# Performance work log

Measured on AMD Instinct MI355X. Metric: run time of the kernel, lower is better.

Reference implementation:

```python
import jax, jax.numpy as jnp
import numpy as np

B, T, D, H = 256, 200, 256, 4
ITEMS = 100000
ALPHA = 0.5
L = 4          # num_blocks: first L//2 causal layers, last L//2 decoder layers
EPS = 1e-8


def _ln(x, s, b):
    m = x.mean(-1, keepdims=True)
    v = ((x - m) ** 2).mean(-1, keepdims=True)
    return (x - m) / jnp.sqrt(v + EPS) * s + b


def _encoder(x, attn_mask, causal_mask, p):
    ln1_s, ln1_b, Wq, bq, Wk, bk, Wv, bv, Wo, bo, ln2_s, ln2_b, W1, b1, W2, b2 = p
    dk = D // H
    Q = _ln(x, ln1_s, ln1_b)
    # attn(Q, seqs, seqs): q from normed input, k/v from raw input
    q = (Q @ Wq + bq).reshape(B, T, H, dk).transpose(0, 2, 1, 3)
    k = (x @ Wk + bk).reshape(B, T, H, dk).transpose(0, 2, 1, 3)
    v = (x @ Wv + bv).reshape(B, T, H, dk).transpose(0, 2, 1, 3)
    scores = jnp.einsum('bhqd,bhkd->bhqk', q, k) / jnp.sqrt(jnp.float32(dk))
    scores = jnp.where(attn_mask[None, None], jnp.float32(-1e9), scores)
    if causal_mask is not None:  # multiplicative reweighting before softmax
        scores = scores * (1.0 + ALPHA * causal_mask[:, None])
    a = jax.nn.softmax(scores, axis=-1)
    o = jnp.einsum('bhqk,bhkd->bhqd', a, v).transpose(0, 2, 1, 3).reshape(B, T, D)
    s = Q + (o @ Wo + bo)          # residual uses normed Q (as in source)
    y = _ln(s, ln2_s, ln2_b)
    return jax.nn.relu(y @ W1 + b1) @ W2 + b2 + y


def setup_inputs() -> dict:
    key = jax.random.key(0)
    ks = jax.random.split(key, 24)
    w = lambda k, shape: jax.random.normal(k, shape, jnp.float32) * 0.02
    log_seqs = jax.random.randint(ks[0], (B, T), 0, ITEMS + 1)
    item_table = w(ks[1], (ITEMS + 1, D)).at[0].set(0.0)   # padding_idx=0
    pos_table = w(ks[2], (T + 1, D)).at[0].set(0.0)        # maxlen+1 rows
    return dict(
        log_seqs=log_seqs,
        item_table=item_table,
        pos_table=pos_table,
        ln1_s=jnp.ones((L, D), jnp.float32), ln1_b=jnp.zeros((L, D), jnp.float32),
        Wq=w(ks[3], (L, D, D)), bq=w(ks[4], (L, D)),
        Wk=w(ks[5], (L, D, D)), bk=w(ks[6], (L, D)),
        Wv=w(ks[7], (L, D, D)), bv=w(ks[8], (L, D)),
        Wo=w(ks[9], (L, D, D)), bo=w(ks[10], (L, D)),
        ln2_s=jnp.ones((L, D), jnp.float32), ln2_b=jnp.zeros((L, D), jnp.float32),
        W1=w(ks[11], (L, D, D)), b1=w(ks[12], (L, D)),
        W2=w(ks[13], (L, D, D)), b2=w(ks[14], (L, D)),
        last_s=jnp.ones((D,), jnp.float32), last_b=jnp.zeros((D,), jnp.float32),
    )


def reference(log_seqs, item_table, pos_table, ln1_s, ln1_b, Wq, bq, Wk, bk, Wv, bv,
              Wo, bo, ln2_s, ln2_b, W1, b1, W2, b2, last_s, last_b):
    seqs = item_table[log_seqs] * jnp.sqrt(jnp.float32(D))
    poss = jnp.arange(1, T + 1)[None, :] * (log_seqs != 0)
    seqs = seqs + pos_table[poss]
    attn_mask = jnp.triu(jnp.ones((T, T), bool), k=1)  # True above diagonal -> masked

    def p(i):
        return (ln1_s[i], ln1_b[i], Wq[i], bq[i], Wk[i], bk[i], Wv[i], bv[i],
                Wo[i], bo[i], ln2_s[i], ln2_b[i], W1[i], b1[i], W2[i], b2[i])

    # causal layers: each applied to the ORIGINAL seqs (matches repo loop)
    causal_z = seqs
    for i in range(L // 2):
        causal_z = _encoder(seqs, attn_mask, None, p(i))
    # batch_cov of causal_z.permute(0,2,1): points [B, N=D, T] -> cov [B, T, T]
    pts = jnp.swapaxes(causal_z, 1, 2)
    diffs = pts - pts.mean(1, keepdims=True)
    causal_mask = jnp.minimum(jnp.einsum('bnt,bns->bts', diffs, diffs) / (D - 1), 3.0)

    x = seqs
    for i in range(L // 2, L):
        x = _encoder(x, attn_mask, causal_mask, p(i))
    return _ln(x, last_s, last_b)
```

## Files before the change

### kernel.cpp

```cpp
#include <hip/hip_runtime.h>
#include <hip/hip_bf16.h>

#define B_ 256
#define T_ 200
#define D_ 256
#define H_ 4
#define BT_ (B_*T_)
#define DD_ (D_*D_)
#define GS_ 72
#define TP_ 208
#define VTP_ 224
#define ZS_ 264
#define FS_ 264
#define VS_ 136

typedef __attribute__((ext_vector_type(4))) float  f32x4;
typedef __attribute__((ext_vector_type(8))) __bf16 bf16x8;
typedef __attribute__((ext_vector_type(4))) int    i32x4;
typedef __attribute__((ext_vector_type(2))) int    i32x2;

union frag8 { unsigned u[4]; bf16x8 v; };

__device__ __forceinline__ unsigned short f2bf(float f) {
    unsigned u = __float_as_uint(f);
    u += 0x7FFFu + ((u >> 16) & 1u);
    return (unsigned short)(u >> 16);
}
__device__ __forceinline__ unsigned pk2(float lo, float hi) {
    return (unsigned)f2bf(lo) | ((unsigned)f2bf(hi) << 16);
}
__device__ __forceinline__ float bflo(unsigned u) { return __uint_as_float(u << 16); }
__device__ __forceinline__ float bfhi(unsigned u) { return __uint_as_float(u & 0xFFFF0000u); }

__device__ __forceinline__ float wave_sum(float v) {
#pragma unroll
    for (int o = 32; o >= 1; o >>= 1) v += __shfl_xor(v, o);
    return v;
}

__global__ void embed_kernel(const int* __restrict__ ls,
                             const float* __restrict__ itab,
                             const float* __restrict__ ptab,
                             unsigned short* __restrict__ seqs) {
    int bt = blockIdx.x;
    int t = bt % T_;
    int lane = threadIdx.x;
    int idx = ls[bt];
    int pos = idx ? (t + 1) : 0;
    float4 a = ((const float4*)(itab + (size_t)idx * D_))[lane];
    float4 p = ((const float4*)(ptab + (size_t)pos * D_))[lane];
    i32x2 r;
    r[0] = (int)pk2(a.x*16.f+p.x, a.y*16.f+p.y);
    r[1] = (int)pk2(a.z*16.f+p.z, a.w*16.f+p.w);
    ((i32x2*)(seqs + (size_t)bt * D_))[lane] = r;
}

template<bool F32OUT>
__global__ __launch_bounds__(256) void ln_kernel(const unsigned short* __restrict__ X,
                                                 const float* __restrict__ sc,
                                                 const float* __restrict__ bi,
                                                 void* __restrict__ Y) {
    int row = blockIdx.x * 4 + (threadIdx.x >> 6);
    int lane = threadIdx.x & 63;
    i32x2 xv = ((const i32x2*)(X + (size_t)row * D_))[lane];
    float x0 = bflo((unsigned)xv[0]), x1 = bfhi((unsigned)xv[0]);
    float x2 = bflo((unsigned)xv[1]), x3 = bfhi((unsigned)xv[1]);
    float m = wave_sum(x0 + x1 + x2 + x3) * (1.f / D_);
    float d0 = x0 - m, d1 = x1 - m, d2 = x2 - m, d3 = x3 - m;
    float v = wave_sum(d0*d0 + d1*d1 + d2*d2 + d3*d3) * (1.f / D_);
    float inv = rsqrtf(v + 1e-8f);
    float4 s4 = ((const float4*)sc)[lane];
    float4 b4 = ((const float4*)bi)[lane];
    float r0 = d0*inv*s4.x + b4.x, r1 = d1*inv*s4.y + b4.y;
    float r2 = d2*inv*s4.z + b4.z, r3 = d3*inv*s4.w + b4.w;
    if (F32OUT) {
        float4 r = {r0, r1, r2, r3};
        ((float4*)Y)[(size_t)row * (D_/4) + lane] = r;
    } else {
        i32x2 r;
        r[0] = (int)pk2(r0, r1);
        r[1] = (int)pk2(r2, r3);
        ((i32x2*)Y)[(size_t)row * (D_/4) + lane] = r;
    }
}

__global__ __launch_bounds__(256) void wtrans_kernel(const float* __restrict__ W,
                                                     unsigned short* __restrict__ Wt) {
    __shared__ float tile[64][65];
    int c0 = blockIdx.x * 64, r0 = blockIdx.y * 64, l = blockIdx.z;
    const float* src = W + (size_t)l * DD_;
    unsigned short* dst = Wt + (size_t)l * DD_;
    int tid = threadIdx.x;
#pragma unroll
    for (int rep = 0; rep < 16; ++rep) {
        int idx = rep * 256 + tid;
        int r = idx >> 6, c = idx & 63;
        tile[r][c] = src[(size_t)(r0 + r) * D_ + c0 + c];
    }
    __syncthreads();
#pragma unroll
    for (int rep = 0; rep < 16; ++rep) {
        int idx = rep * 256 + tid;
        int r2 = idx >> 6, c2 = idx & 63;
        dst[(size_t)(c0 + r2) * D_ + r0 + c2] = f2bf(tile[c2][r2]);
    }
}

__global__ void vtpad_kernel(unsigned short* __restrict__ vt) {
    if (threadIdx.x < VTP_ - T_)
        vt[(size_t)blockIdx.x * VTP_ + T_ + threadIdx.x] = 0;
}

template<int OM, bool RES>
__global__ __launch_bounds__(256) void gemm_mfma(
    const unsigned short* __restrict__ A, const unsigned short* __restrict__ Wt,
    const float* __restrict__ bias, const unsigned short* res,
    unsigned short* Cout) {
    __shared__ unsigned short sh[2 * 128 * GS_];
    unsigned short* As = sh;
    unsigned short* Ws = sh + 128 * GS_;
    int t = threadIdx.x, lane = t & 63, wv = t >> 6;
    int wm = wv >> 1, wn = wv & 1;
    int l15 = lane & 15, l4 = lane >> 4;
    int m0 = blockIdx.y * 128, n0 = blockIdx.x * 128;

    f32x4 acc[4][4];
#pragma unroll
    for (int m = 0; m < 4; ++m)
#pragma unroll
        for (int n = 0; n < 4; ++n)
            acc[m][n] = f32x4{0.f, 0.f, 0.f, 0.f};

    for (int k0 = 0; k0 < D_; k0 += 64) {
#pragma unroll
        for (int rep = 0; rep < 4; ++rep) {
            int idx = rep * 256 + t;
            int r = idx >> 3, c8 = (idx & 7) * 8;
            *(i32x4*)&As[r * GS_ + c8] =
                *(const i32x4*)(A + (size_t)(m0 + r) * D_ + k0 + c8);
        }
#pragma unroll
        for (int rep = 0; rep < 4; ++rep) {
            int idx = rep * 256 + t;
            int r = idx >> 3, c8 = (idx & 7) * 8;
            *(i32x4*)&Ws[r * GS_ + c8] =
                *(const i32x4*)(Wt + (size_t)(n0 + r) * D_ + k0 + c8);
        }
        __syncthreads();
#pragma unroll
        for (int kk = 0; kk < 2; ++kk) {
            bf16x8 af[4], bf[4];
#pragma unroll
            for (int m = 0; m < 4; ++m)
                af[m] = *(const bf16x8*)&As[(wm*64 + m*16 + l15) * GS_ + kk*32 + l4*8];
#pragma unroll
            for (int n = 0; n < 4; ++n)
                bf[n] = *(const bf16x8*)&Ws[(wn*64 + n*16 + l15) * GS_ + kk*32 + l4*8];
#pragma unroll
            for (int m = 0; m < 4; ++m)
#pragma unroll
                for (int n = 0; n < 4; ++n)
                    acc[m][n] = __builtin_amdgcn_mfma_f32_16x16x32_bf16(af[m], bf[n], acc[m][n], 0, 0, 0);
        }
        __syncthreads();
    }

    unsigned short* Ct = sh;
#pragma unroll
    for (int n = 0; n < 4; ++n) {
        int gnl = wn*64 + n*16 + l15;
        int gn = n0 + gnl;
        float bn = bias[gn];
#pragma unroll
        for (int m = 0; m < 4; ++m) {
#pragma unroll
            for (int i = 0; i < 4; ++i) {
                int gml = wm*64 + m*16 + l4*4 + i;
                int gm = m0 + gml;
                float v = acc[m][n][i] + bn;
                if (RES) v += bflo((unsigned)res[(size_t)gm * D_ + gn]);
                Ct[gml * VS_ + gnl] = f2bf(v);
            }
        }
    }
    __syncthreads();
#pragma unroll
    for (int rep = 0; rep < 8; ++rep) {
        int idx = rep * 256 + t;
        int row = idx >> 4, c8 = (idx & 15) * 8;
        int gm = m0 + row;
        i32x4 w = *(const i32x4*)&Ct[row * VS_ + c8];
        if (OM == 0) {
            *(i32x4*)&Cout[(size_t)gm * D_ + n0 + c8] = w;
        } else {
            int b = gm / 200, tt = gm - b * 200;
            *(i32x4*)&Cout[((size_t)b * TP_ + tt) * D_ + n0 + c8] = w;
        }
    }
}

__global__ __launch_bounds__(512) void gemm_kv(
    const unsigned short* __restrict__ A,
    const unsigned short* __restrict__ WtK, const unsigned short* __restrict__ WtV,
    const float* __restrict__ biasK, const float* __restrict__ biasV,
    unsigned short* __restrict__ kbf, unsigned short* __restrict__ vtbf) {
    __shared__ unsigned short sh[3 * 128 * GS_];
    unsigned short* As  = sh;
    unsigned short* WsK = sh + 128 * GS_;
    unsigned short* WsV = sh + 2 * 128 * GS_;
    int t = threadIdx.x, lane = t & 63, wv = t >> 6;
    int wm = wv >> 1, wn = wv & 1;
    int l15 = lane & 15, l4 = lane >> 4;
    int m0 = blockIdx.y * 128, n0 = blockIdx.x * 128;

    f32x4 accK[2][4], accV[2][4];
#pragma unroll
    for (int m = 0; m < 2; ++m)
#pragma unroll
        for (int n = 0; n < 4; ++n) {
            accK[m][n] = f32x4{0.f, 0.f, 0.f, 0.f};
            accV[m][n] = f32x4{0.f, 0.f, 0.f, 0.f};
        }

    for (int k0 = 0; k0 < D_; k0 += 64) {
#pragma unroll
        for (int rep = 0; rep < 2; ++rep) {
            int idx = rep * 512 + t;
            int r = idx >> 3, c8 = (idx & 7) * 8;
            *(i32x4*)&As[r * GS_ + c8]  = *(const i32x4*)(A   + (size_t)(m0 + r) * D_ + k0 + c8);
            *(i32x4*)&WsK[r * GS_ + c8] = *(const i32x4*)(WtK + (size_t)(n0 + r) * D_ + k0 + c8);
            *(i32x4*)&WsV[r * GS_ + c8] = *(const i32x4*)(WtV + (size_t)(n0 + r) * D_ + k0 + c8);
        }
        __syncthreads();
#pragma unroll
        for (int kk = 0; kk < 2; ++kk) {
            bf16x8 af[2];
#pragma unroll
            for (int m = 0; m < 2; ++m)
                af[m] = *(const bf16x8*)&As[(wm*32 + m*16 + l15) * GS_ + kk*32 + l4*8];
#pragma unroll
            for (int n = 0; n < 4; ++n) {
                bf16x8 bk8 = *(const bf16x8*)&WsK[(wn*64 + n*16 + l15) * GS_ + kk*32 + l4*8];
                bf16x8 bv8 = *(const bf16x8*)&WsV[(wn*64 + n*16 + l15) * GS_ + kk*32 + l4*8];
#pragma unroll
                for (int m = 0; m < 2; ++m) {
                    accK[m][n] = __builtin_amdgcn_mfma_f32_16x16x32_bf16(af[m], bk8, accK[m][n], 0, 0, 0);
                    accV[m][n] = __builtin_amdgcn_mfma_f32_16x16x32_bf16(af[m], bv8, accV[m][n], 0, 0, 0);
                }
            }
        }
        __syncthreads();
    }

    unsigned short* Ct = sh;
#pragma unroll
    for (int n = 0; n < 4; ++n) {
        int gnl = wn*64 + n*16 + l15;
        float bnK = biasK[n0 + gnl];
#pragma unroll
        for (int m = 0; m < 2; ++m)
#pragma unroll
            for (int i = 0; i < 4; ++i) {
                int gml = wm*32 + m*16 + l4*4 + i;
                Ct[gml * VS_ + gnl] = f2bf(accK[m][n][i] + bnK);
            }
    }
    __syncthreads();
#pragma unroll
    for (int rep = 0; rep < 4; ++rep) {
        int idx = rep * 512 + t;
        int row = idx >> 4, c8 = (idx & 15) * 8;
        int gm = m0 + row, b = gm / 200, tt = gm - b * 200;
        *(i32x4*)&kbf[((size_t)b * TP_ + tt) * D_ + n0 + c8] =
            *(const i32x4*)&Ct[row * VS_ + c8];
    }
    __syncthreads();

    unsigned short* Vt = sh;
#pragma unroll
    for (int n = 0; n < 4; ++n) {
        int gnl = wn*64 + n*16 + l15;
        float bnV = biasV[n0 + gnl];
#pragma unroll
        for (int m = 0; m < 2; ++m)
#pragma unroll
            for (int i = 0; i < 4; ++i) {
                int gml = wm*32 + m*16 + l4*4 + i;
                Vt[gnl * VS_ + gml] = f2bf(accV[m][n][i] + bnV);
            }
    }
    __syncthreads();
#pragma unroll
    for (int rep = 0; rep < 4; ++rep) {
        int idx = rep * 512 + t;
        int row = idx >> 4, c8 = (idx & 15) * 8;
        int gn = n0 + row, hh = gn >> 6, dk = gn & 63;
        int gm = m0 + c8, b = gm / 200, tt = gm - b * 200;
        *(i32x4*)&vtbf[(((size_t)b * H_ + hh) * 64 + dk) * VTP_ + tt] =
            *(const i32x4*)&Vt[row * VS_ + c8];
    }
}

__global__ __launch_bounds__(256) void ffn_fused(
    const unsigned short* __restrict__ S,
    const float* __restrict__ ln_s, const float* __restrict__ ln_b,
    const unsigned short* __restrict__ Wt1, const float* __restrict__ b1,
    const unsigned short* __restrict__ Wt2, const float* __restrict__ b2,
    unsigned short* __restrict__ OUT) {
    __shared__ unsigned short Alds[32 * FS_];
    __shared__ unsigned short Tlds[32 * FS_];
    __shared__ unsigned short Ws[256 * GS_];
    int t = threadIdx.x, lane = t & 63, wv = t >> 6;
    int l15 = lane & 15, l4 = lane >> 4;
    int m0 = blockIdx.x * 32;

    {
        int r = t >> 3, c = (t & 7) * 32;
        const unsigned short* src = S + (size_t)(m0 + r) * D_ + c;
        i32x4 buf[4];
#pragma unroll
        for (int j = 0; j < 4; ++j) buf[j] = ((const i32x4*)src)[j];
        float sum = 0.f;
#pragma unroll
        for (int j = 0; j < 4; ++j)
#pragma unroll
            for (int q = 0; q < 4; ++q)
                sum += bflo((unsigned)buf[j][q]) + bfhi((unsigned)buf[j][q]);
        sum += __shfl_xor(sum, 1);
        sum += __shfl_xor(sum, 2);
        sum += __shfl_xor(sum, 4);
        float mean = sum * (1.f / D_);
        float var = 0.f;
#pragma unroll
        for (int j = 0; j < 4; ++j)
#pragma unroll
            for (int q = 0; q < 4; ++q) {
                float a0 = bflo((unsigned)buf[j][q]) - mean;
                float a1 = bfhi((unsigned)buf[j][q]) - mean;
                var += a0*a0 + a1*a1;
            }
        var += __shfl_xor(var, 1);
        var += __shfl_xor(var, 2);
        var += __shfl_xor(var, 4);
        float inv = rsqrtf(var * (1.f / D_) + 1e-8f);
#pragma unroll
        for (int j = 0; j < 4; ++j) {
            int cc = c + j * 8;
            float4 sa = *(const float4*)&ln_s[cc];
            float4 sb = *(const float4*)&ln_s[cc + 4];
            float4 ba = *(const float4*)&ln_b[cc];
            float4 bb = *(const float4*)&ln_b[cc + 4];
            float y0 = (bflo((unsigned)buf[j][0]) - mean) * inv * sa.x + ba.x;
            float y1 = (bfhi((unsigned)buf[j][0]) - mean) * inv * sa.y + ba.y;
            float y2 = (bflo((unsigned)buf[j][1]) - mean) * inv * sa.z + ba.z;
            float y3 = (bfhi((unsigned)buf[j][1]) - mean) * inv * sa.w + ba.w;
            float y4 = (bflo((unsigned)buf[j][2]) - mean) * inv * sb.x + bb.x;
            float y5 = (bfhi((unsigned)buf[j][2]) - mean) * inv * sb.y + bb.y;
            float y6 = (bflo((unsigned)buf[j][3]) - mean) * inv * sb.z + bb.z;
            float y7 = (bfhi((unsigned)buf[j][3]) - mean) * inv * sb.w + bb.w;
            i32x4 w;
            w[0] = (int)pk2(y0, y1);
            w[1] = (int)pk2(y2, y3);
            w[2] = (int)pk2(y4, y5);
            w[3] = (int)pk2(y6, y7);
            *(i32x4*)&Alds[r * FS_ + cc] = w;
        }
    }
    __syncthreads();

    f32x4 acc[2][4];
#pragma unroll
    for (int m = 0; m < 2; ++m)
#pragma unroll
        for (int n = 0; n < 4; ++n)
            acc[m][n] = f32x4{0.f, 0.f, 0.f, 0.f};
    for (int k0 = 0; k0 < D_; k0 += 64) {
#pragma unroll
        for (int rep = 0; rep < 8; ++rep) {
            int idx = rep * 256 + t;
            int rr = idx >> 3, c8 = (idx & 7) * 8;
            *(i32x4*)&Ws[rr * GS_ + c8] = *(const i32x4*)(Wt1 + (size_t)rr * D_ + k0 + c8);
        }
        __syncthreads();
#pragma unroll
        for (int kk = 0; kk < 2; ++kk) {
            bf16x8 af[2], bf[4];
#pragma unroll
            for (int m = 0; m < 2; ++m)
                af[m] = *(const bf16x8*)&Alds[(m*16 + l15) * FS_ + k0 + kk*32 + l4*8];
#pragma unroll
            for (int n = 0; n < 4; ++n)
                bf[n] = *(const bf16x8*)&Ws[(wv*64 + n*16 + l15) * GS_ + kk*32 + l4*8];
#pragma unroll
            for (int m = 0; m < 2; ++m)
#pragma unroll
                for (int n = 0; n < 4; ++n)
                    acc[m][n] = __builtin_amdgcn_mfma_f32_16x16x32_bf16(af[m], bf[n], acc[m][n], 0, 0, 0);
        }
        __syncthreads();
    }
#pragma unroll
    for (int n = 0; n < 4; ++n) {
        int gn = wv*64 + n*16 + l15;
        float bn = b1[gn];
#pragma unroll
        for (int m = 0; m < 2; ++m)
#pragma unroll
            for (int i = 0; i < 4; ++i)
                Tlds[(m*16 + l4*4 + i) * FS_ + gn] = f2bf(fmaxf(acc[m][n][i] + bn, 0.f));
    }
    __syncthreads();

#pragma unroll
    for (int m = 0; m < 2; ++m)
#pragma unroll
        for (int n = 0; n < 4; ++n)
            acc[m][n] = f32x4{0.f, 0.f, 0.f, 0.f};
    for (int k0 = 0; k0 < D_; k0 += 64) {
#pragma unroll
        for (int rep = 0; rep < 8; ++rep) {
            int idx = rep * 256 + t;
            int rr = idx >> 3, c8 = (idx & 7) * 8;
            *(i32x4*)&Ws[rr * GS_ + c8] = *(const i32x4*)(Wt2 + (size_t)rr * D_ + k0 + c8);
        }
        __syncthreads();
#pragma unroll
        for (int kk = 0; kk < 2; ++kk) {
            bf16x8 af[2], bf[4];
#pragma unroll
            for (int m = 0; m < 2; ++m)
                af[m] = *(const bf16x8*)&Tlds[(m*16 + l15) * FS_ + k0 + kk*32 + l4*8];
#pragma unroll
            for (int n = 0; n < 4; ++n)
                bf[n] = *(const bf16x8*)&Ws[(wv*64 + n*16 + l15) * GS_ + kk*32 + l4*8];
#pragma unroll
            for (int m = 0; m < 2; ++m)
#pragma unroll
                for (int n = 0; n < 4; ++n)
                    acc[m][n] = __builtin_amdgcn_mfma_f32_16x16x32_bf16(af[m], bf[n], acc[m][n], 0, 0, 0);
        }
        __syncthreads();
    }
#pragma unroll
    for (int n = 0; n < 4; ++n) {
        int gn = wv*64 + n*16 + l15;
        float bn = b2[gn];
#pragma unroll
        for (int m = 0; m < 2; ++m) {
#pragma unroll
            for (int i = 0; i < 4; ++i) {
                int row = m*16 + l4*4 + i;
                float v = acc[m][n][i] + bn + bflo((unsigned)Alds[row * FS_ + gn]);
                Tlds[row * FS_ + gn] = f2bf(v);
            }
        }
    }
    __syncthreads();
#pragma unroll
    for (int rep = 0; rep < 4; ++rep) {
        int idx = rep * 256 + t;
        int row = idx >> 5, c8 = (idx & 31) * 8;
        *(i32x4*)&OUT[(size_t)(m0 + row) * D_ + c8] = *(const i32x4*)&Tlds[row * FS_ + c8];
    }
}

template<bool DEC>
__global__ __launch_bounds__(64) void attn_mfma(
    const unsigned short* __restrict__ qbf,
    const unsigned short* __restrict__ kbf,
    const unsigned short* __restrict__ vtbf,
    const float* __restrict__ cm,
    unsigned short* __restrict__ obf) {
    __shared__ unsigned short Olds[16 * 72];
    int o = ((blockIdx.x & 7) * 1664) + (blockIdx.x >> 3);
    int b = o / 52;
    int r = o - b * 52;
    int h = r / 13;
    int qt = r - h * 13;
    int lane = threadIdx.x;
    int l15 = lane & 15, l4 = lane >> 4;
    int q0 = qt * 16;
    int qr = q0 + l15;
    const f32x4 zero = {0.f, 0.f, 0.f, 0.f};

    size_t qkb = ((size_t)b * TP_) * D_ + h * 64;
    const unsigned short* qp = qbf + qkb + (size_t)(q0 + l15) * D_ + l4 * 8;
    bf16x8 bq0 = *(const bf16x8*)qp;
    bf16x8 bq1 = *(const bf16x8*)(qp + 32);

    size_t vbase = ((size_t)(b * H_ + h)) * 64 * VTP_;
    int sA = l15 + ((l4 & 1) << 5);
    int sB = sA + 16;
    bool lo4 = (l4 < 2);

    float m = -3e38f, l = 0.f;
    f32x4 O[4] = {zero, zero, zero, zero};

    int npair = (qt >> 1) + 1;
    for (int p = 0; p < npair; ++p) {
        int kt0 = 2 * p;
        bool hasOdd = (kt0 + 1 <= qt);

        f32x4 sv0, sv1;
        {
            const unsigned short* kp = kbf + qkb + (size_t)(kt0 * 16 + l15) * D_ + l4 * 8;
            bf16x8 ak0 = *(const bf16x8*)kp;
            bf16x8 ak1 = *(const bf16x8*)(kp + 32);
            __builtin_amdgcn_s_setprio(1);
            f32x4 acc = __builtin_amdgcn_mfma_f32_16x16x32_bf16(ak0, bq0, zero, 0, 0, 0);
            acc = __builtin_amdgcn_mfma_f32_16x16x32_bf16(ak1, bq1, acc, 0, 0, 0);
            __builtin_amdgcn_s_setprio(0);
#pragma unroll
            for (int i = 0; i < 4; ++i) {
                int kk = kt0 * 16 + l4 * 4 + i;
                float s = acc[i] * 0.125f;
                bool vld = (qr < T_) && (kk < T_);
                float cmv = (DEC && vld) ? cm[((size_t)(b * T_) + kk) * T_ + qr] : 0.f;
                if (!vld) s = -1e9f;
                else {
                    if (kk > qr) s = -1e9f;
                    if (DEC) s *= (1.0f + 0.5f * cmv);
                }
                sv0[i] = s;
            }
        }
        if (hasOdd) {
            const unsigned short* kp = kbf + qkb + (size_t)((kt0 + 1) * 16 + l15) * D_ + l4 * 8;
            bf16x8 ak0 = *(const bf16x8*)kp;
            bf16x8 ak1 = *(const bf16x8*)(kp + 32);
            __builtin_amdgcn_s_setprio(1);
            f32x4 acc = __builtin_amdgcn_mfma_f32_16x16x32_bf16(ak0, bq0, zero, 0, 0, 0);
            acc = __builtin_amdgcn_mfma_f32_16x16x32_bf16(ak1, bq1, acc, 0, 0, 0);
            __builtin_amdgcn_s_setprio(0);
#pragma unroll
            for (int i = 0; i < 4; ++i) {
                int kk = (kt0 + 1) * 16 + l4 * 4 + i;
                float s = acc[i] * 0.125f;
                bool vld = (qr < T_) && (kk < T_);
                float cmv = (DEC && vld) ? cm[((size_t)(b * T_) + kk) * T_ + qr] : 0.f;
                if (!vld) s = -1e9f;
                else {
                    if (kk > qr) s = -1e9f;
                    if (DEC) s *= (1.0f + 0.5f * cmv);
                }
                sv1[i] = s;
            }
        }

        float tm = fmaxf(fmaxf(sv0[0], sv0[1]), fmaxf(sv0[2], sv0[3]));
        if (hasOdd) {
            float tm1 = fmaxf(fmaxf(sv1[0], sv1[1]), fmaxf(sv1[2], sv1[3]));
            tm = fmaxf(tm, tm1);
        }
        tm = fmaxf(tm, __shfl_xor(tm, 16));
        tm = fmaxf(tm, __shfl_xor(tm, 32));
        float m_new = fmaxf(m, tm);
        float sc = __expf(m - m_new);
        m = m_new;
        l *= sc;
#pragma unroll
        for (int i = 0; i < 4; ++i) {
            float osc = __shfl(sc, l4 * 4 + i);
#pragma unroll
            for (int dt = 0; dt < 4; ++dt) O[dt][i] *= osc;
        }

        float p0[4], p1[4];
#pragma unroll
        for (int i = 0; i < 4; ++i) {
            p0[i] = __expf(sv0[i] - m);
            l += p0[i];
        }
        if (hasOdd) {
#pragma unroll
            for (int i = 0; i < 4; ++i) {
                p1[i] = __expf(sv1[i] - m);
                l += p1[i];
            }
        } else {
#pragma unroll
            for (int i = 0; i < 4; ++i) p1[i] = 0.f;
        }

        unsigned pk0a = pk2(p0[0], p0[1]), pk0b = pk2(p0[2], p0[3]);
        unsigned pk1a = pk2(p1[0], p1[1]), pk1b = pk2(p1[2], p1[3]);
        unsigned e0 = (unsigned)__shfl((int)pk0a, sA);
        unsigned e1 = (unsigned)__shfl((int)pk0b, sA);
        unsigned e2 = (unsigned)__shfl((int)pk0a, sB);
        unsigned e3 = (unsigned)__shfl((int)pk0b, sB);
        unsigned o0 = (unsigned)__shfl((int)pk1a, sA);
        unsigned o1 = (unsigned)__shfl((int)pk1b, sA);
        unsigned o2 = (unsigned)__shfl((int)pk1a, sB);
        unsigned o3 = (unsigned)__shfl((int)pk1b, sB);
        frag8 pa;
        pa.u[0] = lo4 ? e0 : o0;
        pa.u[1] = lo4 ? e1 : o1;
        pa.u[2] = lo4 ? e2 : o2;
        pa.u[3] = lo4 ? e3 : o3;

        __builtin_amdgcn_s_setprio(1);
#pragma unroll
        for (int dt = 0; dt < 4; ++dt) {
            bf16x8 vf = *(const bf16x8*)&vtbf[vbase + (size_t)(dt * 16 + l15) * VTP_ + p * 32 + l4 * 8];
            O[dt] = __builtin_amdgcn_mfma_f32_16x16x32_bf16(pa.v, vf, O[dt], 0, 0, 0);
        }
        __builtin_amdgcn_s_setprio(0);
    }

    float L = l;
    L += __shfl_xor(L, 16);
    L += __shfl_xor(L, 32);
    float inv = 1.f / L;
#pragma unroll
    for (int i = 0; i < 4; ++i) {
        float oin = __shfl(inv, l4 * 4 + i);
#pragma unroll
        for (int dt = 0; dt < 4; ++dt)
            Olds[(l4 * 4 + i) * 72 + dt * 16 + l15] = f2bf(O[dt][i] * oin);
    }
    __syncthreads();
#pragma unroll
    for (int rep = 0; rep < 2; ++rep) {
        int idx = rep * 64 + lane;
        int row = idx >> 3, c8 = (idx & 7) * 8;
        int qrow = q0 + row;
        if (qrow < T_)
            *(i32x4*)&obf[((size_t)(b * T_) + qrow) * D_ + h * 64 + c8] =
                *(const i32x4*)&Olds[row * 72 + c8];
    }
}

__global__ __launch_bounds__(512) void cov_mfma(const unsigned short* __restrict__ Z,
                                                float* __restrict__ cm) {
    __shared__ unsigned short Zb[208 * ZS_];
    int b = blockIdx.x;
    int tid = threadIdx.x, lane = tid & 63, wv = tid >> 6;
    int l15 = lane & 15, l4 = lane >> 4;

    for (int i = tid; i < T_ * 64; i += 512) {
        int t = i >> 6, c4 = (i & 63) << 2;
        i32x2 z = *(const i32x2*)(Z + ((size_t)b * T_ + t) * D_ + c4);
        float z0 = bflo((unsigned)z[0]), z1 = bfhi((unsigned)z[0]);
        float z2 = bflo((unsigned)z[1]), z3 = bfhi((unsigned)z[1]);
        float mean = wave_sum(z0 + z1 + z2 + z3) * (1.f / D_);
        unsigned* p = (unsigned*)&Zb[t * ZS_ + c4];
        p[0] = pk2(z0 - mean, z1 - mean);
        p[1] = pk2(z2 - mean, z3 - mean);
    }
    for (int i = tid; i < 8 * ZS_; i += 512) Zb[T_ * ZS_ + i] = 0;
    __syncthreads();

    for (int job = wv; job < 91; job += 8) {
        int ti = 0;
        while ((ti + 1) * (ti + 2) / 2 <= job) ++ti;
        int tj = job - ti * (ti + 1) / 2;
        f32x4 acc = {0.f, 0.f, 0.f, 0.f};
#pragma unroll
        for (int s = 0; s < 8; ++s) {
            bf16x8 a  = *(const bf16x8*)&Zb[(ti * 16 + l15) * ZS_ + s * 32 + l4 * 8];
            bf16x8 bb = *(const bf16x8*)&Zb[(tj * 16 + l15) * ZS_ + s * 32 + l4 * 8];
            acc = __builtin_amdgcn_mfma_f32_16x16x32_bf16(a, bb, acc, 0, 0, 0);
        }
#pragma unroll
        for (int i = 0; i < 4; ++i) {
            int t = ti * 16 + l4 * 4 + i, s2 = tj * 16 + l15;
            float vv = fminf(acc[i] * (1.f / 255.f), 3.0f);
            if (t < T_ && s2 < T_) {
                cm[((size_t)b * T_ + t) * T_ + s2] = vv;
                cm[((size_t)b * T_ + s2) * T_ + t] = vv;
            }
        }
    }
}

extern "C" void kernel_launch(void* const* d_in, const int* in_sizes, int n_in,
                              void* d_out, int out_size, void* d_ws, size_t ws_size,
                              hipStream_t stream) {
    const int*   log_seqs = (const int*)  d_in[0];
    const float* item_tab = (const float*)d_in[1];
    const float* pos_tab  = (const float*)d_in[2];
    const float* ln1_s = (const float*)d_in[3];
    const float* ln1_b = (const float*)d_in[4];
    const float* Wq = (const float*)d_in[5];
    const float* bq = (const float*)d_in[6];
    const float* Wk = (const float*)d_in[7];
    const float* bk = (const float*)d_in[8];
    const float* Wv = (const float*)d_in[9];
    const float* bv = (const float*)d_in[10];
    const float* Wo = (const float*)d_in[11];
    const float* bo = (const float*)d_in[12];
    const float* ln2_s = (const float*)d_in[13];
    const float* ln2_b = (const float*)d_in[14];
    const float* W1 = (const float*)d_in[15];
    const float* b1 = (const float*)d_in[16];
    const float* W2 = (const float*)d_in[17];
    const float* b2 = (const float*)d_in[18];
    const float* last_s = (const float*)d_in[19];
    const float* last_b = (const float*)d_in[20];

    const size_t NTD = (size_t)BT_ * D_;
    float* cmask = (float*)d_ws;
    unsigned short* act = (unsigned short*)(cmask + (size_t)B_ * T_ * T_);
    unsigned short* s0   = act;
    unsigned short* s1   = s0 + NTD;
    unsigned short* Qn   = s1 + NTD;
    unsigned short* vb   = Qn + NTD;
    unsigned short* qbf  = vb + NTD;
    unsigned short* kbf  = qbf + (size_t)B_ * TP_ * D_;
    unsigned short* vtbf = kbf + (size_t)B_ * TP_ * D_;
    unsigned short* wtb  = vtbf + (size_t)B_ * H_ * 64 * VTP_;

    unsigned short* wtq = wtb;
    unsigned short* wtk = wtb + 4 * (size_t)DD_;
    unsigned short* wtv = wtb + 8 * (size_t)DD_;
    unsigned short* wto = wtb + 12 * (size_t)DD_;
    unsigned short* wt1 = wtb + 16 * (size_t)DD_;
    unsigned short* wt2 = wtb + 20 * (size_t)DD_;

    dim3 tg(4, 4, 4);
    wtrans_kernel<<<tg, 256, 0, stream>>>(Wq, wtq);
    wtrans_kernel<<<tg, 256, 0, stream>>>(Wk, wtk);
    wtrans_kernel<<<tg, 256, 0, stream>>>(Wv, wtv);
    wtrans_kernel<<<tg, 256, 0, stream>>>(Wo, wto);
    wtrans_kernel<<<tg, 256, 0, stream>>>(W1, wt1);
    wtrans_kernel<<<tg, 256, 0, stream>>>(W2, wt2);
    vtpad_kernel<<<B_ * H_ * 64, 32, 0, stream>>>(vtbf);

    dim3 gg(2, 400);

    auto encoder = [&](const unsigned short* X, unsigned short* OUT, int i, const float* cmp) {
        ln_kernel<false><<<BT_/4, 256, 0, stream>>>(X, ln1_s + i*D_, ln1_b + i*D_, Qn);
        gemm_mfma<1,false><<<gg, 256, 0, stream>>>(Qn, wtq + (size_t)i*DD_, bq + i*D_, nullptr, qbf);
        gemm_kv<<<gg, 512, 0, stream>>>(X, wtk + (size_t)i*DD_, wtv + (size_t)i*DD_,
                                        bk + i*D_, bv + i*D_, kbf, vtbf);
        if (cmp) attn_mfma<true ><<<13312, 64, 0, stream>>>(qbf, kbf, vtbf, cmp, vb);
        else     attn_mfma<false><<<13312, 64, 0, stream>>>(qbf, kbf, vtbf, nullptr, vb);
        gemm_mfma<0,true><<<gg, 256, 0, stream>>>(vb, wto + (size_t)i*DD_, bo + i*D_, Qn, Qn);
        ffn_fused<<<BT_/32, 256, 0, stream>>>(Qn, ln2_s + i*D_, ln2_b + i*D_,
                                              wt1 + (size_t)i*DD_, b1 + i*D_,
                                              wt2 + (size_t)i*DD_, b2 + i*D_, OUT);
    };

    embed_kernel<<<BT_, 64, 0, stream>>>(log_seqs, item_tab, pos_tab, s0);

    encoder(s0, s1, 1, nullptr);

    cov_mfma<<<B_, 512, 0, stream>>>(s1, cmask);

    encoder(s0, s1, 2, cmask);
    encoder(s1, s0, 3, cmask);

    ln_kernel<true><<<BT_/4, 256, 0, stream>>>(s0, last_s, last_b, (float*)d_out);
}
```

Measured before the change: 784.4 us.

## Pair short and long causal query tiles per attention wave; widen GEMM blocks

The attention kernel now gives each 64-thread block two query tiles, j and 12-j. Their causal work sums to a constant, which balances load and lets the two tiles share the K and V fragment loads per key-tile pair. Separately, the 128x128 GEMM now runs 512 threads with 8 waves, each computing a 32x64 sub-tile, so each wave has fewer accumulators. The costs are more live registers in the attention kernel for two sets of accumulators, and more serialized work per block.

```diff
diff --git a/kernel.cpp b/kernel.cpp
--- a/kernel.cpp
+++ b/kernel.cpp
@@ -112,7 +112,7 @@
 }
 
 template<int OM, bool RES>
-__global__ __launch_bounds__(256) void gemm_mfma(
+__global__ __launch_bounds__(512) void gemm_mfma(
     const unsigned short* __restrict__ A, const unsigned short* __restrict__ Wt,
     const float* __restrict__ bias, const unsigned short* res,
     unsigned short* Cout) {
@@ -124,40 +124,33 @@
     int l15 = lane & 15, l4 = lane >> 4;
     int m0 = blockIdx.y * 128, n0 = blockIdx.x * 128;
 
-    f32x4 acc[4][4];
-#pragma unroll
-    for (int m = 0; m < 4; ++m)
+    f32x4 acc[2][4];
+#pragma unroll
+    for (int m = 0; m < 2; ++m)
 #pragma unroll
         for (int n = 0; n < 4; ++n)
             acc[m][n] = f32x4{0.f, 0.f, 0.f, 0.f};
 
     for (int k0 = 0; k0 < D_; k0 += 64) {
 #pragma unroll
-        for (int rep = 0; rep < 4; ++rep) {
-            int idx = rep * 256 + t;
+        for (int rep = 0; rep < 2; ++rep) {
+            int idx = rep * 512 + t;
             int r = idx >> 3, c8 = (idx & 7) * 8;
-            *(i32x4*)&As[r * GS_ + c8] =
-                *(const i32x4*)(A + (size_t)(m0 + r) * D_ + k0 + c8);
-        }
-#pragma unroll
-        for (int rep = 0; rep < 4; ++rep) {
-            int idx = rep * 256 + t;
-            int r = idx >> 3, c8 = (idx & 7) * 8;
-            *(i32x4*)&Ws[r * GS_ + c8] =
-                *(const i32x4*)(Wt + (size_t)(n0 + r) * D_ + k0 + c8);
+            *(i32x4*)&As[r * GS_ + c8] = *(const i32x4*)(A  + (size_t)(m0 + r) * D_ + k0 + c8);
+            *(i32x4*)&Ws[r * GS_ + c8] = *(const i32x4*)(Wt + (size_t)(n0 + r) * D_ + k0 + c8);
         }
         __syncthreads();
 #pragma unroll
         for (int kk = 0; kk < 2; ++kk) {
-            bf16x8 af[4], bf[4];
-#pragma unroll
-            for (int m = 0; m < 4; ++m)
-                af[m] = *(const bf16x8*)&As[(wm*64 + m*16 + l15) * GS_ + kk*32 + l4*8];
+            bf16x8 af[2], bf[4];
+#pragma unroll
+            for (int m = 0; m < 2; ++m)
+                af[m] = *(const bf16x8*)&As[(wm*32 + m*16 + l15) * GS_ + kk*32 + l4*8];
 #pragma unroll
             for (int n = 0; n < 4; ++n)
                 bf[n] = *(const bf16x8*)&Ws[(wn*64 + n*16 + l15) * GS_ + kk*32 + l4*8];
 #pragma unroll
-            for (int m = 0; m < 4; ++m)
+            for (int m = 0; m < 2; ++m)
 #pragma unroll
                 for (int n = 0; n < 4; ++n)
                     acc[m][n] = __builtin_amdgcn_mfma_f32_16x16x32_bf16(af[m], bf[n], acc[m][n], 0, 0, 0);
@@ -172,10 +165,10 @@
         int gn = n0 + gnl;
         float bn = bias[gn];
 #pragma unroll
-        for (int m = 0; m < 4; ++m) {
+        for (int m = 0; m < 2; ++m) {
 #pragma unroll
             for (int i = 0; i < 4; ++i) {
-                int gml = wm*64 + m*16 + l4*4 + i;
+                int gml = wm*32 + m*16 + l4*4 + i;
                 int gm = m0 + gml;
                 float v = acc[m][n][i] + bn;
                 if (RES) v += bflo((unsigned)res[(size_t)gm * D_ + gn]);
@@ -185,8 +178,8 @@
     }
     __syncthreads();
 #pragma unroll
-    for (int rep = 0; rep < 8; ++rep) {
-        int idx = rep * 256 + t;
+    for (int rep = 0; rep < 4; ++rep) {
+        int idx = rep * 512 + t;
         int row = idx >> 4, c8 = (idx & 15) * 8;
         int gm = m0 + row;
         i32x4 w = *(const i32x4*)&Ct[row * VS_ + c8];
@@ -465,168 +458,260 @@
 }
 
 template<bool DEC>
+__device__ __forceinline__ f32x4 score_ep(f32x4 acc, int kt, int qr, int l4,
+                                          size_t bT, const float* __restrict__ cm) {
+    f32x4 sv;
+#pragma unroll
+    for (int i = 0; i < 4; ++i) {
+        int kk = kt * 16 + l4 * 4 + i;
+        float s = acc[i] * 0.125f;
+        bool vld = (qr < T_) && (kk < T_);
+        float cmv = (DEC && vld) ? cm[(bT + kk) * T_ + qr] : 0.f;
+        if (!vld) s = -1e9f;
+        else {
+            if (kk > qr) s = -1e9f;
+            if (DEC) s *= (1.0f + 0.5f * cmv);
+        }
+        sv[i] = s;
+    }
+    return sv;
+}
+
+template<bool DEC>
 __global__ __launch_bounds__(64) void attn_mfma(
     const unsigned short* __restrict__ qbf,
     const unsigned short* __restrict__ kbf,
     const unsigned short* __restrict__ vtbf,
     const float* __restrict__ cm,
     unsigned short* __restrict__ obf) {
-    __shared__ unsigned short Olds[16 * 72];
-    int o = ((blockIdx.x & 7) * 1664) + (blockIdx.x >> 3);
-    int b = o / 52;
-    int r = o - b * 52;
-    int h = r / 13;
-    int qt = r - h * 13;
+    __shared__ unsigned short Olds[32 * 72];
+    int o = ((blockIdx.x & 7) * 896) + (blockIdx.x >> 3);
+    int b = o / 28;
+    int r = o - b * 28;
+    int h = r / 7;
+    int j = r - h * 7;
+    int qtA = j, qtB = 12 - j;
+    bool hasA = (qtA != qtB);
     int lane = threadIdx.x;
     int l15 = lane & 15, l4 = lane >> 4;
-    int q0 = qt * 16;
-    int qr = q0 + l15;
+    int q0A = qtA * 16, q0B = qtB * 16;
+    int qrA = q0A + l15, qrB = q0B + l15;
+    size_t bT = (size_t)b * T_;
     const f32x4 zero = {0.f, 0.f, 0.f, 0.f};
 
     size_t qkb = ((size_t)b * TP_) * D_ + h * 64;
-    const unsigned short* qp = qbf + qkb + (size_t)(q0 + l15) * D_ + l4 * 8;
-    bf16x8 bq0 = *(const bf16x8*)qp;
-    bf16x8 bq1 = *(const bf16x8*)(qp + 32);
+    const unsigned short* qpB = qbf + qkb + (size_t)(q0B + l15) * D_ + l4 * 8;
+    bf16x8 bqB0 = *(const bf16x8*)qpB;
+    bf16x8 bqB1 = *(const bf16x8*)(qpB + 32);
+    bf16x8 bqA0 = bqB0, bqA1 = bqB1;
+    if (hasA) {
+        const unsigned short* qpA = qbf + qkb + (size_t)(q0A + l15) * D_ + l4 * 8;
+        bqA0 = *(const bf16x8*)qpA;
+        bqA1 = *(const bf16x8*)(qpA + 32);
+    }
 
     size_t vbase = ((size_t)(b * H_ + h)) * 64 * VTP_;
     int sA = l15 + ((l4 & 1) << 5);
     int sB = sA + 16;
     bool lo4 = (l4 < 2);
 
-    float m = -3e38f, l = 0.f;
-    f32x4 O[4] = {zero, zero, zero, zero};
-
-    int npair = (qt >> 1) + 1;
+    float mA = -3e38f, lA = 0.f, mB = -3e38f, lB = 0.f;
+    f32x4 OA[4] = {zero, zero, zero, zero};
+    f32x4 OB[4] = {zero, zero, zero, zero};
+
+    int npair = (qtB >> 1) + 1;
     for (int p = 0; p < npair; ++p) {
         int kt0 = 2 * p;
-        bool hasOdd = (kt0 + 1 <= qt);
-
-        f32x4 sv0, sv1;
+        bool oddB = (kt0 + 1 <= qtB);
+        bool evnA = hasA && (kt0 <= qtA);
+        bool oddA = hasA && (kt0 + 1 <= qtA);
+
+        const unsigned short* kp0 = kbf + qkb + (size_t)(kt0 * 16 + l15) * D_ + l4 * 8;
+        bf16x8 ak00 = *(const bf16x8*)kp0;
+        bf16x8 ak01 = *(const bf16x8*)(kp0 + 32);
+        bf16x8 ak10 = ak00, ak11 = ak01;
+        if (oddB) {
+            const unsigned short* kp1 = kp0 + (size_t)16 * D_;
+            ak10 = *(const bf16x8*)kp1;
+            ak11 = *(const bf16x8*)(kp1 + 32);
+        }
+
+        f32x4 svB0, svB1, svA0, svA1;
         {
-            const unsigned short* kp = kbf + qkb + (size_t)(kt0 * 16 + l15) * D_ + l4 * 8;
-            bf16x8 ak0 = *(const bf16x8*)kp;
-            bf16x8 ak1 = *(const bf16x8*)(kp + 32);
             __builtin_amdgcn_s_setprio(1);
-            f32x4 acc = __builtin_amdgcn_mfma_f32_16x16x32_bf16(ak0, bq0, zero, 0, 0, 0);
-            acc = __builtin_amdgcn_mfma_f32_16x16x32_bf16(ak1, bq1, acc, 0, 0, 0);
+            f32x4 acc = __builtin_amdgcn_mfma_f32_16x16x32_bf16(ak00, bqB0, zero, 0, 0, 0);
+            acc = __builtin_amdgcn_mfma_f32_16x16x32_bf16(ak01, bqB1, acc, 0, 0, 0);
             __builtin_amdgcn_s_setprio(0);
+            svB0 = score_ep<DEC>(acc, kt0, qrB, l4, bT, cm);
+        }
+        if (oddB) {
+            __builtin_amdgcn_s_setprio(1);
+            f32x4 acc = __builtin_amdgcn_mfma_f32_16x16x32_bf16(ak10, bqB0, zero, 0, 0, 0);
+            acc = __builtin_amdgcn_mfma_f32_16x16x32_bf16(ak11, bqB1, acc, 0, 0, 0);
+            __builtin_amdgcn_s_setprio(0);
+            svB1 = score_ep<DEC>(acc, kt0 + 1, qrB, l4, bT, cm);
+        }
+        if (evnA) {
+            __builtin_amdgcn_s_setprio(1);
+            f32x4 acc = __builtin_amdgcn_mfma_f32_16x16x32_bf16(ak00, bqA0, zero, 0, 0, 0);
+            acc = __builtin_amdgcn_mfma_f32_16x16x32_bf16(ak01, bqA1, acc, 0, 0, 0);
+            __builtin_amdgcn_s_setprio(0);
+            svA0 = score_ep<DEC>(acc, kt0, qrA, l4, bT, cm);
+        }
+        if (oddA) {
+            __builtin_amdgcn_s_setprio(1);
+            f32x4 acc = __builtin_amdgcn_mfma_f32_16x16x32_bf16(ak10, bqA0, zero, 0, 0, 0);
+            acc = __builtin_amdgcn_mfma_f32_16x16x32_bf16(ak11, bqA1, acc, 0, 0, 0);
+            __builtin_amdgcn_s_setprio(0);
+            svA1 = score_ep<DEC>(acc, kt0 + 1, qrA, l4, bT, cm);
+        }
+
+        bf16x8 vf[4];
+#pragma unroll
+        for (int dt = 0; dt < 4; ++dt)
+            vf[dt] = *(const bf16x8*)&vtbf[vbase + (size_t)(dt * 16 + l15) * VTP_ + p * 32 + l4 * 8];
+
+        {
+            float tm = fmaxf(fmaxf(svB0[0], svB0[1]), fmaxf(svB0[2], svB0[3]));
+            if (oddB) tm = fmaxf(tm, fmaxf(fmaxf(svB1[0], svB1[1]), fmaxf(svB1[2], svB1[3])));
+            tm = fmaxf(tm, __shfl_xor(tm, 16));
+            tm = fmaxf(tm, __shfl_xor(tm, 32));
+            float mn = fmaxf(mB, tm);
+            float sc = __expf(mB - mn);
+            mB = mn;
+            lB *= sc;
 #pragma unroll
             for (int i = 0; i < 4; ++i) {
-                int kk = kt0 * 16 + l4 * 4 + i;
-                float s = acc[i] * 0.125f;
-                bool vld = (qr < T_) && (kk < T_);
-                float cmv = (DEC && vld) ? cm[((size_t)(b * T_) + kk) * T_ + qr] : 0.f;
-                if (!vld) s = -1e9f;
-                else {
-                    if (kk > qr) s = -1e9f;
-                    if (DEC) s *= (1.0f + 0.5f * cmv);
-                }
-                sv0[i] = s;
-            }
-        }
-        if (hasOdd) {
-            const unsigned short* kp = kbf + qkb + (size_t)((kt0 + 1) * 16 + l15) * D_ + l4 * 8;
-            bf16x8 ak0 = *(const bf16x8*)kp;
-            bf16x8 ak1 = *(const bf16x8*)(kp + 32);
+                float osc = __shfl(sc, l4 * 4 + i);
+#pragma unroll
+                for (int dt = 0; dt < 4; ++dt) OB[dt][i] *= osc;
+            }
+            float p0[4], p1[4];
+#pragma unroll
+            for (int i = 0; i < 4; ++i) { p0[i] = __expf(svB0[i] - mB); lB += p0[i]; }
+            if (oddB) {
+#pragma unroll
+                for (int i = 0; i < 4; ++i) { p1[i] = __expf(svB1[i] - mB); lB += p1[i]; }
+            } else {
+#pragma unroll
+                for (int i = 0; i < 4; ++i) p1[i] = 0.f;
+            }
+            unsigned pk0a = pk2(p0[0], p0[1]), pk0b = pk2(p0[2], p0[3]);
+            unsigned pk1a = pk2(p1[0], p1[1]), pk1b = pk2(p1[2], p1[3]);
+            unsigned e0 = (unsigned)__shfl((int)pk0a, sA);
+            unsigned e1 = (unsigned)__shfl((int)pk0b, sA);
+            unsigned e2 = (unsigned)__shfl((int)pk0a, sB);
+            unsigned e3 = (unsigned)__shfl((int)pk0b, sB);
+            unsigned o0 = (unsigned)__shfl((int)pk1a, sA);
+            unsigned o1 = (unsigned)__shfl((int)pk1b, sA);
+            unsigned o2 = (unsigned)__shfl((int)pk1a, sB);
+            unsigned o3 = (unsigned)__shfl((int)pk1b, sB);
+            frag8 pa;
+            pa.u[0] = lo4 ? e0 : o0;
+            pa.u[1] = lo4 ? e1 : o1;
+            pa.u[2] = lo4 ? e2 : o2;
+            pa.u[3] = lo4 ? e3 : o3;
             __builtin_amdgcn_s_setprio(1);
-            f32x4 acc = __builtin_amdgcn_mfma_f32_16x16x32_bf16(ak0, bq0, zero, 0, 0, 0);
-            acc = __builtin_amdgcn_mfma_f32_16x16x32_bf16(ak1, bq1, acc, 0, 0, 0);
+#pragma unroll
+            for (int dt = 0; dt < 4; ++dt)
+                OB[dt] = __builtin_amdgcn_mfma_f32_16x16x32_bf16(pa.v, vf[dt], OB[dt], 0, 0, 0);
             __builtin_amdgcn_s_setprio(0);
+        }
+
+        if (evnA) {
+            float tm = fmaxf(fmaxf(svA0[0], svA0[1]), fmaxf(svA0[2], svA0[3]));
+            if (oddA) tm = fmaxf(tm, fmaxf(fmaxf(svA1[0], svA1[1]), fmaxf(svA1[2], svA1[3])));
+            tm = fmaxf(tm, __shfl_xor(tm, 16));
+            tm = fmaxf(tm, __shfl_xor(tm, 32));
+            float mn = fmaxf(mA, tm);
+            float sc = __expf(mA - mn);
+            mA = mn;
+            lA *= sc;
 #pragma unroll
             for (int i = 0; i < 4; ++i) {
-                int kk = (kt0 + 1) * 16 + l4 * 4 + i;
-                float s = acc[i] * 0.125f;
-                bool vld = (qr < T_) && (kk < T_);
-                float cmv = (DEC && vld) ? cm[((size_t)(b * T_) + kk) * T_ + qr] : 0.f;
-                if (!vld) s = -1e9f;
-                else {
-                    if (kk > qr) s = -1e9f;
-                    if (DEC) s *= (1.0f + 0.5f * cmv);
-                }
-                sv1[i] = s;
-            }
-        }
-
-        float tm = fmaxf(fmaxf(sv0[0], sv0[1]), fmaxf(sv0[2], sv0[3]));
-        if (hasOdd) {
-            float tm1 = fmaxf(fmaxf(sv1[0], sv1[1]), fmaxf(sv1[2], sv1[3]));
-            tm = fmaxf(tm, tm1);
-        }
-        tm = fmaxf(tm, __shfl_xor(tm, 16));
-        tm = fmaxf(tm, __shfl_xor(tm, 32));
-        float m_new = fmaxf(m, tm);
-        float sc = __expf(m - m_new);
-        m = m_new;
-        l *= sc;
+                float osc = __shfl(sc, l4 * 4 + i);
+#pragma unroll
+                for (int dt = 0; dt < 4; ++dt) OA[dt][i] *= osc;
+            }
+            float p0[4], p1[4];
+#pragma unroll
+            for (int i = 0; i < 4; ++i) { p0[i] = __expf(svA0[i] - mA); lA += p0[i]; }
+            if (oddA) {
+#pragma unroll
+                for (int i = 0; i < 4; ++i) { p1[i] = __expf(svA1[i] - mA); lA += p1[i]; }
+            } else {
+#pragma unroll
+                for (int i = 0; i < 4; ++i) p1[i] = 0.f;
+            }
+            unsigned pk0a = pk2(p0[0], p0[1]), pk0b = pk2(p0[2], p0[3]);
+            unsigned pk1a = pk2(p1[0], p1[1]), pk1b = pk2(p1[2], p1[3]);
+            unsigned e0 = (unsigned)__shfl((int)pk0a, sA);
+            unsigned e1 = (unsigned)__shfl((int)pk0b, sA);
+            unsigned e2 = (unsigned)__shfl((int)pk0a, sB);
+            unsigned e3 = (unsigned)__shfl((int)pk0b, sB);
+            unsigned o0 = (unsigned)__shfl((int)pk1a, sA);
+            unsigned o1 = (unsigned)__shfl((int)pk1b, sA);
+            unsigned o2 = (unsigned)__shfl((int)pk1a, sB);
+            unsigned o3 = (unsigned)__shfl((int)pk1b, sB);
+            frag8 pa;
+            pa.u[0] = lo4 ? e0 : o0;
+            pa.u[1] = lo4 ? e1 : o1;
+            pa.u[2] = lo4 ? e2 : o2;
+            pa.u[3] = lo4 ? e3 : o3;
+            __builtin_amdgcn_s_setprio(1);
+#pragma unroll
+            for (int dt = 0; dt < 4; ++dt)
+                OA[dt] = __builtin_amdgcn_mfma_f32_16x16x32_bf16(pa.v, vf[dt], OA[dt], 0, 0, 0);
+            __builtin_amdgcn_s_setprio(0);
+        }
+    }
+
+    {
+        float L = lB;
+        L += __shfl_xor(L, 16);
+        L += __shfl_xor(L, 32);
+        float inv = 1.f / L;
 #pragma unroll
         for (int i = 0; i < 4; ++i) {
-            float osc = __shfl(sc, l4 * 4 + i);
-#pragma unroll
-            for (int dt = 0; dt < 4; ++dt) O[dt][i] *= osc;
-        }
-
-        float p0[4], p1[4];
+            float oin = __shfl(inv, l4 * 4 + i);
+#pragma unroll
+            for (int dt = 0; dt < 4; ++dt)
+                Olds[(l4 * 4 + i) * 72 + dt * 16 + l15] = f2bf(OB[dt][i] * oin);
+        }
+    }
+    if (hasA) {
+        float L = lA;
+        L += __shfl_xor(L, 16);
+        L += __shfl_xor(L, 32);
+        float inv = 1.f / L;
 #pragma unroll
         for (int i = 0; i < 4; ++i) {
-            p0[i] = __expf(sv0[i] - m);
-            l += p0[i];
-        }
-        if (hasOdd) {
-#pragma unroll
-            for (int i = 0; i < 4; ++i) {
-                p1[i] = __expf(sv1[i] - m);
-                l += p1[i];
-            }
-        } else {
-#pragma unroll
-            for (int i = 0; i < 4; ++i) p1[i] = 0.f;
-        }
-
-        unsigned pk0a = pk2(p0[0], p0[1]), pk0b = pk2(p0[2], p0[3]);
-        unsigned pk1a = pk2(p1[0], p1[1]), pk1b = pk2(p1[2], p1[3]);
-        unsigned e0 = (unsigned)__shfl((int)pk0a, sA);
-        unsigned e1 = (unsigned)__shfl((int)pk0b, sA);
-        unsigned e2 = (unsigned)__shfl((int)pk0a, sB);
-        unsigned e3 = (unsigned)__shfl((int)pk0b, sB);
-        unsigned o0 = (unsigned)__shfl((int)pk1a, sA);
-        unsigned o1 = (unsigned)__shfl((int)pk1b, sA);
-        unsigned o2 = (unsigned)__shfl((int)pk1a, sB);
-        unsigned o3 = (unsigned)__shfl((int)pk1b, sB);
-        frag8 pa;
-        pa.u[0] = lo4 ? e0 : o0;
-        pa.u[1] = lo4 ? e1 : o1;
-        pa.u[2] = lo4 ? e2 : o2;
-        pa.u[3] = lo4 ? e3 : o3;
-
-        __builtin_amdgcn_s_setprio(1);
-#pragma unroll
-        for (int dt = 0; dt < 4; ++dt) {
-            bf16x8 vf = *(const bf16x8*)&vtbf[vbase + (size_t)(dt * 16 + l15) * VTP_ + p * 32 + l4 * 8];
-            O[dt] = __builtin_amdgcn_mfma_f32_16x16x32_bf16(pa.v, vf, O[dt], 0, 0, 0);
-        }
-        __builtin_amdgcn_s_setprio(0);
-    }
-
-    float L = l;
-    L += __shfl_xor(L, 16);
-    L += __shfl_xor(L, 32);
-    float inv = 1.f / L;
-#pragma unroll
-    for (int i = 0; i < 4; ++i) {
-        float oin = __shfl(inv, l4 * 4 + i);
-#pragma unroll
-        for (int dt = 0; dt < 4; ++dt)
-            Olds[(l4 * 4 + i) * 72 + dt * 16 + l15] = f2bf(O[dt][i] * oin);
+            float oin = __shfl(inv, l4 * 4 + i);
+#pragma unroll
+            for (int dt = 0; dt < 4; ++dt)
+                Olds[(16 + l4 * 4 + i) * 72 + dt * 16 + l15] = f2bf(OA[dt][i] * oin);
+        }
     }
     __syncthreads();
 #pragma unroll
     for (int rep = 0; rep < 2; ++rep) {
         int idx = rep * 64 + lane;
         int row = idx >> 3, c8 = (idx & 7) * 8;
-        int qrow = q0 + row;
+        int qrow = q0B + row;
         if (qrow < T_)
-            *(i32x4*)&obf[((size_t)(b * T_) + qrow) * D_ + h * 64 + c8] =
+            *(i32x4*)&obf[(bT + qrow) * D_ + h * 64 + c8] =
                 *(const i32x4*)&Olds[row * 72 + c8];
+    }
+    if (hasA) {
+#pragma unroll
+        for (int rep = 0; rep < 2; ++rep) {
+            int idx = rep * 64 + lane;
+            int row = idx >> 3, c8 = (idx & 7) * 8;
+            int qrow = q0A + row;
+            if (qrow < T_)
+                *(i32x4*)&obf[(bT + qrow) * D_ + h * 64 + c8] =
+                    *(const i32x4*)&Olds[(16 + row) * 72 + c8];
+        }
     }
 }
 
@@ -730,12 +815,12 @@
 
     auto encoder = [&](const unsigned short* X, unsigned short* OUT, int i, const float* cmp) {
         ln_kernel<false><<<BT_/4, 256, 0, stream>>>(X, ln1_s + i*D_, ln1_b + i*D_, Qn);
-        gemm_mfma<1,false><<<gg, 256, 0, stream>>>(Qn, wtq + (size_t)i*DD_, bq + i*D_, nullptr, qbf);
+        gemm_mfma<1,false><<<gg, 512, 0, stream>>>(Qn, wtq + (size_t)i*DD_, bq + i*D_, nullptr, qbf);
         gemm_kv<<<gg, 512, 0, stream>>>(X, wtk + (size_t)i*DD_, wtv + (size_t)i*DD_,
                                         bk + i*D_, bv + i*D_, kbf, vtbf);
-        if (cmp) attn_mfma<true ><<<13312, 64, 0, stream>>>(qbf, kbf, vtbf, cmp, vb);
-        else     attn_mfma<false><<<13312, 64, 0, stream>>>(qbf, kbf, vtbf, nullptr, vb);
-        gemm_mfma<0,true><<<gg, 256, 0, stream>>>(vb, wto + (size_t)i*DD_, bo + i*D_, Qn, Qn);
+        if (cmp) attn_mfma<true ><<<7168, 64, 0, stream>>>(qbf, kbf, vtbf, cmp, vb);
+        else     attn_mfma<false><<<7168, 64, 0, stream>>>(qbf, kbf, vtbf, nullptr, vb);
+        gemm_mfma<0,true><<<gg, 512, 0, stream>>>(vb, wto + (size_t)i*DD_, bo + i*D_, Qn, Qn);
         ffn_fused<<<BT_/32, 256, 0, stream>>>(Qn, ln2_s + i*D_, ln2_b + i*D_,
                                               wt1 + (size_t)i*DD_, b1 + i*D_,
                                               wt2 + (size_t)i*DD_, b2 + i*D_, OUT);
```

After: 714.1 us. -9.0%, faster.
